# Kernel tuning notes

Hardware: AMD Instinct MI355X
Metric: run time of the kernel (lower is better)

## Reference

```python
import jax, jax.numpy as jnp
import numpy as np


def setup_inputs() -> dict:
    key = jax.random.key(0)
    k1, k2, k3, k4 = jax.random.split(key, 4)
    in_f, out_f, rank, tokens = 4096, 4096, 256, 8192
    bound = 1.0 / np.sqrt(in_f)
    x = jax.random.normal(k1, (tokens, in_f), dtype=jnp.float32)
    U = jax.random.uniform(k2, (out_f, rank), dtype=jnp.float32, minval=-bound, maxval=bound)
    V = jax.random.uniform(k3, (rank, in_f), dtype=jnp.float32, minval=-bound, maxval=bound)
    bias = jax.random.uniform(k4, (out_f,), dtype=jnp.float32, minval=-bound, maxval=bound)
    return {"x": x, "U": U, "V": V, "bias": bias}


def reference(x, U, V, bias):
    # Faithful to original: materialize W = U @ V, then F.linear(x, W, bias) = x @ W.T + bias
    W = U @ V                      # [out, in]
    return x @ W.T + bias          # [tokens, out]
```

## Files before the change

kernel.cpp:

```cpp
#include <hip/hip_runtime.h>
#include <stdint.h>

#define TOKENS 8192
#define INF    4096
#define OUTF   4096
#define RANK   256

typedef __attribute__((ext_vector_type(8))) short bf16x8;
typedef __attribute__((ext_vector_type(4))) float f32x4;

__device__ __forceinline__ unsigned short f2bf(float f) {
    union { float f; unsigned int u; } v; v.f = f;
    unsigned int r = v.u + 0x7FFFu + ((v.u >> 16) & 1u);
    return (unsigned short)(r >> 16);
}

__device__ __forceinline__ void gl_lds16(const void* g, void* l) {
    __builtin_amdgcn_global_load_lds(
        (const __attribute__((address_space(1))) unsigned int*)g,
        (__attribute__((address_space(3))) unsigned int*)l, 16, 0, 0);
}

__global__ void cvt4(const float4* __restrict__ in, ushort4* __restrict__ out) {
    int i = blockIdx.x * blockDim.x + threadIdx.x;
    float4 v = in[i];
    ushort4 o;
    o.x = f2bf(v.x); o.y = f2bf(v.y); o.z = f2bf(v.z); o.w = f2bf(v.w);
    out[i] = o;
}

#define G1_BM 32
#define G1_BK 128
#define A1_STR 136

__device__ __forceinline__ void g1_loadV(bf16x8 (&V)[2][4],
                                         const unsigned short* vr0,
                                         const unsigned short* vr1,
                                         int kk, int quad) {
    #pragma unroll
    for (int ks = 0; ks < 4; ++ks) {
        V[0][ks] = *(const bf16x8*)(vr0 + kk + ks * 32 + quad * 8);
        V[1][ks] = *(const bf16x8*)(vr1 + kk + ks * 32 + quad * 8);
    }
}

__device__ __forceinline__ void g1_compute(f32x4 (&acc)[2][2],
                                           const bf16x8 (&V)[2][4],
                                           const unsigned short* ax,
                                           int l15, int quad) {
    #pragma unroll
    for (int ks = 0; ks < 4; ++ks) {
        bf16x8 b0 = *(const bf16x8*)(ax + l15 * A1_STR + ks * 32 + quad * 8);
        bf16x8 b1 = *(const bf16x8*)(ax + (16 + l15) * A1_STR + ks * 32 + quad * 8);
        acc[0][0] = __builtin_amdgcn_mfma_f32_16x16x32_bf16(V[0][ks], b0, acc[0][0], 0, 0, 0);
        acc[0][1] = __builtin_amdgcn_mfma_f32_16x16x32_bf16(V[0][ks], b1, acc[0][1], 0, 0, 0);
        acc[1][0] = __builtin_amdgcn_mfma_f32_16x16x32_bf16(V[1][ks], b0, acc[1][0], 0, 0, 0);
        acc[1][1] = __builtin_amdgcn_mfma_f32_16x16x32_bf16(V[1][ks], b1, acc[1][1], 0, 0, 0);
    }
}

__device__ __forceinline__ void g1_pack(float4 a, float4 b, unsigned short* dst) {
    union { bf16x8 v; unsigned short s[8]; } pk;
    pk.s[0] = f2bf(a.x); pk.s[1] = f2bf(a.y);
    pk.s[2] = f2bf(a.z); pk.s[3] = f2bf(a.w);
    pk.s[4] = f2bf(b.x); pk.s[5] = f2bf(b.y);
    pk.s[6] = f2bf(b.z); pk.s[7] = f2bf(b.w);
    *(bf16x8*)dst = pk.v;
}

__global__ __launch_bounds__(512) void gemm1(const float* __restrict__ x,
                                             const unsigned short* __restrict__ Vb,
                                             unsigned short* __restrict__ T) {
    __shared__ __align__(16) unsigned short Ax[2][G1_BM * A1_STR];

    const int tid  = threadIdx.x;
    const int lane = tid & 63;
    const int wid  = tid >> 6;
    const int m0   = blockIdx.x * G1_BM;
    const int l15  = lane & 15;
    const int quad = lane >> 4;

    const int arow = tid >> 4;
    const int aseg = tid & 15;
    const float* xp = x + (size_t)(m0 + arow) * INF + aseg * 8;
    unsigned short* aw0 = &Ax[0][arow * A1_STR + aseg * 8];
    unsigned short* aw1 = &Ax[1][arow * A1_STR + aseg * 8];

    const unsigned short* vr0 = Vb + (size_t)(wid * 32 + l15) * INF;
    const unsigned short* vr1 = vr0 + (size_t)16 * INF;

    f32x4 acc[2][2];
    #pragma unroll
    for (int i = 0; i < 2; ++i)
        #pragma unroll
        for (int j = 0; j < 2; ++j) acc[i][j] = (f32x4){0.f, 0.f, 0.f, 0.f};

    bf16x8 VA[2][4], VB[2][4];

    float4 xr0 = *(const float4*)(xp);
    float4 xr1 = *(const float4*)(xp + 4);
    g1_pack(xr0, xr1, aw0);
    g1_loadV(VA, vr0, vr1, 0, quad);

    for (int kt = 0; kt < 32; kt += 2) {
        const int k1 = (kt + 1) * G1_BK;
        const int k2 = (kt + 2 < 32 ? kt + 2 : 31) * G1_BK;

        __syncthreads();
        xr0 = *(const float4*)(xp + k1);
        xr1 = *(const float4*)(xp + k1 + 4);
        g1_loadV(VB, vr0, vr1, k1, quad);
        g1_compute(acc, VA, &Ax[0][0], l15, quad);
        g1_pack(xr0, xr1, aw1);

        __syncthreads();
        xr0 = *(const float4*)(xp + k2);
        xr1 = *(const float4*)(xp + k2 + 4);
        g1_loadV(VA, vr0, vr1, k2, quad);
        g1_compute(acc, VB, &Ax[1][0], l15, quad);
        g1_pack(xr0, xr1, aw0);
    }

    #pragma unroll
    for (int mv = 0; mv < 2; ++mv) {
        #pragma unroll
        for (int mx = 0; mx < 2; ++mx) {
            int m = m0 + mx * 16 + l15;
            int n = wid * 32 + mv * 16 + quad * 4;
            ushort4 o;
            o.x = f2bf(acc[mv][mx][0]); o.y = f2bf(acc[mv][mx][1]);
            o.z = f2bf(acc[mv][mx][2]); o.w = f2bf(acc[mv][mx][3]);
            *(ushort4*)&T[(size_t)m * RANK + n] = o;
        }
    }
}

#define G2_BM 128
#define G2_BN 128
#define G2_BK 64

__device__ __forceinline__ void g2_stage(unsigned short (&Tl)[2][G2_BM * G2_BK],
                                         unsigned short (&Ul)[2][G2_BN * G2_BK],
                                         int b, int kk,
                                         const unsigned short* Tb,
                                         const unsigned short* Ub,
                                         int m0, int n0, int wid, int lrow, int cf) {
    #pragma unroll
    for (int j = 0; j < 4; ++j) {
        int r0 = wid * 32 + j * 8;
        gl_lds16(Tb + (size_t)(m0 + r0 + lrow) * RANK + kk + cf * 8, &Tl[b][r0 * G2_BK]);
        gl_lds16(Ub + (size_t)(n0 + r0 + lrow) * RANK + kk + cf * 8, &Ul[b][r0 * G2_BK]);
    }
}

__global__ __launch_bounds__(256) void gemm2(const unsigned short* __restrict__ Tb,
                                             const unsigned short* __restrict__ Ub,
                                             const float* __restrict__ bias,
                                             float* __restrict__ out) {
    __shared__ __align__(16) unsigned short Tlds[2][G2_BM * G2_BK];
    __shared__ __align__(16) unsigned short Ulds[2][G2_BN * G2_BK];

    const int tid  = threadIdx.x;
    const int lane = tid & 63;
    const int wid  = tid >> 6;
    const int wy   = wid >> 1, wx = wid & 1;
    const int m0   = blockIdx.y * G2_BM;
    const int n0   = blockIdx.x * G2_BN;
    const int l15  = lane & 15, quad = lane >> 4;
    const int lrow = lane >> 3;
    const int cf   = (lane & 7) ^ lrow;

    f32x4 acc[4][4];
    #pragma unroll
    for (int i = 0; i < 4; i++)
        #pragma unroll
        for (int j = 0; j < 4; j++) acc[i][j] = (f32x4){0.f, 0.f, 0.f, 0.f};

    float4 bv[4];
    #pragma unroll
    for (int nt = 0; nt < 4; ++nt)
        bv[nt] = *(const float4*)&bias[n0 + wx * 64 + nt * 16 + quad * 4];

    g2_stage(Tlds, Ulds, 0, 0, Tb, Ub, m0, n0, wid, lrow, cf);

    #pragma unroll
    for (int t = 0; t < 4; ++t) {
        __syncthreads();
        if (t < 3)
            g2_stage(Tlds, Ulds, (t + 1) & 1, (t + 1) * G2_BK,
                     Tb, Ub, m0, n0, wid, lrow, cf);
        const int b = t & 1;
        #pragma unroll
        for (int ks = 0; ks < 2; ++ks) {
            bf16x8 aU[4], bT[4];
            #pragma unroll
            for (int tt = 0; tt < 4; ++tt) {
                int ur = wx * 64 + tt * 16 + l15;
                int up = (ks * 4 + quad) ^ (ur & 7);
                aU[tt] = *(const bf16x8*)&Ulds[b][ur * G2_BK + up * 8];
                int tr = wy * 64 + tt * 16 + l15;
                int tp = (ks * 4 + quad) ^ (tr & 7);
                bT[tt] = *(const bf16x8*)&Tlds[b][tr * G2_BK + tp * 8];
            }
            #pragma unroll
            for (int nt = 0; nt < 4; ++nt)
                #pragma unroll
                for (int mt = 0; mt < 4; ++mt)
                    acc[nt][mt] = __builtin_amdgcn_mfma_f32_16x16x32_bf16(
                        aU[nt], bT[mt], acc[nt][mt], 0, 0, 0);
        }
    }

    #pragma unroll
    for (int nt = 0; nt < 4; ++nt) {
        int n_base = n0 + wx * 64 + nt * 16 + quad * 4;
        #pragma unroll
        for (int mt = 0; mt < 4; ++mt) {
            int m = m0 + wy * 64 + mt * 16 + l15;
            float4 v;
            v.x = acc[nt][mt][0] + bv[nt].x;
            v.y = acc[nt][mt][1] + bv[nt].y;
            v.z = acc[nt][mt][2] + bv[nt].z;
            v.w = acc[nt][mt][3] + bv[nt].w;
            *(float4*)&out[(size_t)m * OUTF + n_base] = v;
        }
    }
}

extern "C" void kernel_launch(void* const* d_in, const int* in_sizes, int n_in,
                              void* d_out, int out_size, void* d_ws, size_t ws_size,
                              hipStream_t stream) {
    const float* x    = (const float*)d_in[0];
    const float* U    = (const float*)d_in[1];
    const float* V    = (const float*)d_in[2];
    const float* bias = (const float*)d_in[3];
    float* out = (float*)d_out;

    unsigned short* Vb = (unsigned short*)d_ws;
    unsigned short* Ub = Vb + (size_t)RANK * INF;
    unsigned short* Tb = Ub + (size_t)OUTF * RANK;

    cvt4<<<(RANK * INF / 4) / 256, 256, 0, stream>>>((const float4*)V, (ushort4*)Vb);
    cvt4<<<(OUTF * RANK / 4) / 256, 256, 0, stream>>>((const float4*)U, (ushort4*)Ub);
    gemm1<<<TOKENS / G1_BM, 512, 0, stream>>>(x, Vb, Tb);
    gemm2<<<dim3(OUTF / G2_BN, TOKENS / G2_BM), 256, 0, stream>>>(Tb, Ub, bias, out);
}
```

Baseline: 300.3 us.

## Stage V tiles through swizzled LDS with async global-to-LDS loads; merge conversions

In gemm1, V tiles now go through double-buffered LDS using global_load_lds with an XOR swizzle, instead of per-lane register loads straight from global memory. The loop is restructured with an explicit tail. The two fp32-to-bf16 conversion launches are also merged into a single kernel to save one launch. LDS use rises to about 145KB per block (two 64KB V buffers plus the A buffers), which limits occupancy to one block per CU and may exceed the LDS limit.

After: 284.2 us. 1.06x faster.

```diff
diff --git a/kernel.cpp b/kernel.cpp
--- a/kernel.cpp
+++ b/kernel.cpp
@@ -21,41 +21,29 @@
         (__attribute__((address_space(3))) unsigned int*)l, 16, 0, 0);
 }
 
-__global__ void cvt4(const float4* __restrict__ in, ushort4* __restrict__ out) {
+__global__ void cvt4(const float4* __restrict__ va, ushort4* __restrict__ oa, int na,
+                     const float4* __restrict__ vb, ushort4* __restrict__ ob) {
     int i = blockIdx.x * blockDim.x + threadIdx.x;
-    float4 v = in[i];
+    float4 v;
+    if (i < na) v = va[i]; else v = vb[i - na];
     ushort4 o;
     o.x = f2bf(v.x); o.y = f2bf(v.y); o.z = f2bf(v.z); o.w = f2bf(v.w);
-    out[i] = o;
+    if (i < na) oa[i] = o; else ob[i - na] = o;
 }
 
 #define G1_BM 32
 #define G1_BK 128
 #define A1_STR 136
 
-__device__ __forceinline__ void g1_loadV(bf16x8 (&V)[2][4],
-                                         const unsigned short* vr0,
-                                         const unsigned short* vr1,
-                                         int kk, int quad) {
-    #pragma unroll
-    for (int ks = 0; ks < 4; ++ks) {
-        V[0][ks] = *(const bf16x8*)(vr0 + kk + ks * 32 + quad * 8);
-        V[1][ks] = *(const bf16x8*)(vr1 + kk + ks * 32 + quad * 8);
-    }
-}
-
-__device__ __forceinline__ void g1_compute(f32x4 (&acc)[2][2],
-                                           const bf16x8 (&V)[2][4],
-                                           const unsigned short* ax,
-                                           int l15, int quad) {
-    #pragma unroll
-    for (int ks = 0; ks < 4; ++ks) {
-        bf16x8 b0 = *(const bf16x8*)(ax + l15 * A1_STR + ks * 32 + quad * 8);
-        bf16x8 b1 = *(const bf16x8*)(ax + (16 + l15) * A1_STR + ks * 32 + quad * 8);
-        acc[0][0] = __builtin_amdgcn_mfma_f32_16x16x32_bf16(V[0][ks], b0, acc[0][0], 0, 0, 0);
-        acc[0][1] = __builtin_amdgcn_mfma_f32_16x16x32_bf16(V[0][ks], b1, acc[0][1], 0, 0, 0);
-        acc[1][0] = __builtin_amdgcn_mfma_f32_16x16x32_bf16(V[1][ks], b0, acc[1][0], 0, 0, 0);
-        acc[1][1] = __builtin_amdgcn_mfma_f32_16x16x32_bf16(V[1][ks], b1, acc[1][1], 0, 0, 0);
+__device__ __forceinline__ void g1_stageV(const unsigned short* __restrict__ Vb,
+                                          unsigned short* vdst, int kk,
+                                          int wid, int lane) {
+    #pragma unroll
+    for (int j = 0; j < 8; ++j) {
+        int r0  = wid * 32 + j * 4;
+        int row = r0 + (lane >> 4);
+        int c   = (lane & 15) ^ (row & 7);
+        gl_lds16(Vb + (size_t)row * INF + kk + c * 8, vdst + r0 * G1_BK);
     }
 }
 
@@ -68,10 +56,33 @@
     *(bf16x8*)dst = pk.v;
 }
 
+__device__ __forceinline__ void g1_compute(f32x4 (&acc)[2][2],
+                                           const unsigned short* vbuf,
+                                           const unsigned short* abuf,
+                                           int l15, int quad, int wid) {
+    const int rr0 = wid * 32 + l15;
+    const int sw  = l15 & 7;
+    #pragma unroll
+    for (int ks = 0; ks < 4; ++ks) {
+        int p = ((ks * 4 + quad) ^ sw) * 8;
+        bf16x8 v0 = *(const bf16x8*)&vbuf[rr0 * G1_BK + p];
+        bf16x8 v1 = *(const bf16x8*)&vbuf[(rr0 + 16) * G1_BK + p];
+        bf16x8 b0 = *(const bf16x8*)&abuf[l15 * A1_STR + ks * 32 + quad * 8];
+        bf16x8 b1 = *(const bf16x8*)&abuf[(16 + l15) * A1_STR + ks * 32 + quad * 8];
+        acc[0][0] = __builtin_amdgcn_mfma_f32_16x16x32_bf16(v0, b0, acc[0][0], 0, 0, 0);
+        acc[0][1] = __builtin_amdgcn_mfma_f32_16x16x32_bf16(v0, b1, acc[0][1], 0, 0, 0);
+        acc[1][0] = __builtin_amdgcn_mfma_f32_16x16x32_bf16(v1, b0, acc[1][0], 0, 0, 0);
+        acc[1][1] = __builtin_amdgcn_mfma_f32_16x16x32_bf16(v1, b1, acc[1][1], 0, 0, 0);
+    }
+}
+
 __global__ __launch_bounds__(512) void gemm1(const float* __restrict__ x,
                                              const unsigned short* __restrict__ Vb,
                                              unsigned short* __restrict__ T) {
-    __shared__ __align__(16) unsigned short Ax[2][G1_BM * A1_STR];
+    __shared__ __align__(16) unsigned short V0[RANK * G1_BK];
+    __shared__ __align__(16) unsigned short V1[RANK * G1_BK];
+    __shared__ __align__(16) unsigned short A0[G1_BM * A1_STR];
+    __shared__ __align__(16) unsigned short A1[G1_BM * A1_STR];
 
     const int tid  = threadIdx.x;
     const int lane = tid & 63;
@@ -83,11 +94,8 @@
     const int arow = tid >> 4;
     const int aseg = tid & 15;
     const float* xp = x + (size_t)(m0 + arow) * INF + aseg * 8;
-    unsigned short* aw0 = &Ax[0][arow * A1_STR + aseg * 8];
-    unsigned short* aw1 = &Ax[1][arow * A1_STR + aseg * 8];
-
-    const unsigned short* vr0 = Vb + (size_t)(wid * 32 + l15) * INF;
-    const unsigned short* vr1 = vr0 + (size_t)16 * INF;
+    unsigned short* aw0 = &A0[arow * A1_STR + aseg * 8];
+    unsigned short* aw1 = &A1[arow * A1_STR + aseg * 8];
 
     f32x4 acc[2][2];
     #pragma unroll
@@ -95,31 +103,34 @@
         #pragma unroll
         for (int j = 0; j < 2; ++j) acc[i][j] = (f32x4){0.f, 0.f, 0.f, 0.f};
 
-    bf16x8 VA[2][4], VB[2][4];
-
+    g1_stageV(Vb, V0, 0, wid, lane);
     float4 xr0 = *(const float4*)(xp);
     float4 xr1 = *(const float4*)(xp + 4);
     g1_pack(xr0, xr1, aw0);
-    g1_loadV(VA, vr0, vr1, 0, quad);
-
-    for (int kt = 0; kt < 32; kt += 2) {
-        const int k1 = (kt + 1) * G1_BK;
-        const int k2 = (kt + 2 < 32 ? kt + 2 : 31) * G1_BK;
-
+
+    for (int t = 0; t < 30; t += 2) {
         __syncthreads();
-        xr0 = *(const float4*)(xp + k1);
-        xr1 = *(const float4*)(xp + k1 + 4);
-        g1_loadV(VB, vr0, vr1, k1, quad);
-        g1_compute(acc, VA, &Ax[0][0], l15, quad);
+        g1_stageV(Vb, V1, (t + 1) * G1_BK, wid, lane);
+        xr0 = *(const float4*)(xp + (t + 1) * G1_BK);
+        xr1 = *(const float4*)(xp + (t + 1) * G1_BK + 4);
+        g1_compute(acc, V0, A0, l15, quad, wid);
         g1_pack(xr0, xr1, aw1);
 
         __syncthreads();
-        xr0 = *(const float4*)(xp + k2);
-        xr1 = *(const float4*)(xp + k2 + 4);
-        g1_loadV(VA, vr0, vr1, k2, quad);
-        g1_compute(acc, VB, &Ax[1][0], l15, quad);
+        g1_stageV(Vb, V0, (t + 2) * G1_BK, wid, lane);
+        xr0 = *(const float4*)(xp + (t + 2) * G1_BK);
+        xr1 = *(const float4*)(xp + (t + 2) * G1_BK + 4);
+        g1_compute(acc, V1, A1, l15, quad, wid);
         g1_pack(xr0, xr1, aw0);
     }
+    __syncthreads();
+    g1_stageV(Vb, V1, 31 * G1_BK, wid, lane);
+    xr0 = *(const float4*)(xp + 31 * G1_BK);
+    xr1 = *(const float4*)(xp + 31 * G1_BK + 4);
+    g1_compute(acc, V0, A0, l15, quad, wid);
+    g1_pack(xr0, xr1, aw1);
+    __syncthreads();
+    g1_compute(acc, V1, A1, l15, quad, wid);
 
     #pragma unroll
     for (int mv = 0; mv < 2; ++mv) {
@@ -240,8 +251,10 @@
     unsigned short* Ub = Vb + (size_t)RANK * INF;
     unsigned short* Tb = Ub + (size_t)OUTF * RANK;
 
-    cvt4<<<(RANK * INF / 4) / 256, 256, 0, stream>>>((const float4*)V, (ushort4*)Vb);
-    cvt4<<<(OUTF * RANK / 4) / 256, 256, 0, stream>>>((const float4*)U, (ushort4*)Ub);
+    const int nv = RANK * INF / 4;
+    const int nu = OUTF * RANK / 4;
+    cvt4<<<(nv + nu) / 256, 256, 0, stream>>>((const float4*)V, (ushort4*)Vb, nv,
+                                              (const float4*)U, (ushort4*)Ub);
     gemm1<<<TOKENS / G1_BM, 512, 0, stream>>>(x, Vb, Tb);
     gemm2<<<dim3(OUTF / G2_BN, TOKENS / G2_BM), 256, 0, stream>>>(Tb, Ub, bias, out);
 }
```
